# Performance work log

Hardware: AMD Instinct MI355X
Metric: run time of the kernel (lower is better)

The kernel has to match this reference:

```python
import jax, jax.numpy as jnp
import numpy as np

EPS = 1e-5

def _bn(x, g, b, m, v):
    # eval-mode batchnorm over channel axis 1 of NCHW
    scale = g * jax.lax.rsqrt(v + EPS)
    return x * scale[None, :, None, None] + (b - m * scale)[None, :, None, None]

def _dwconv3x3(x, w):
    # x: [N,C,H,W], w: [C,1,3,3] depthwise, stride 1, pad 1
    C = x.shape[1]
    return jax.lax.conv_general_dilated(
        x, w, window_strides=(1, 1), padding=((1, 1), (1, 1)),
        dimension_numbers=('NCHW', 'OIHW', 'NCHW'), feature_group_count=C)

def setup_inputs() -> dict:
    key = jax.random.key(0)
    ks = jax.random.split(key, 16)
    N, C, H, W = 32, 96, 56, 56
    Hd = 576  # hidden_dim = round(96 * 6)
    inp = {}
    inp['x'] = jax.random.normal(ks[0], (N, C, H, W), jnp.float32)
    inp['w1'] = jax.random.normal(ks[1], (Hd, C), jnp.float32) * 0.05
    inp['g1'] = jax.random.uniform(ks[2], (Hd,), jnp.float32, 0.5, 1.5)
    inp['b1'] = jax.random.normal(ks[3], (Hd,), jnp.float32) * 0.1
    inp['m1'] = jax.random.normal(ks[4], (Hd,), jnp.float32) * 0.1
    inp['v1'] = jax.random.uniform(ks[5], (Hd,), jnp.float32, 0.5, 1.5)
    inp['wdw'] = jax.random.normal(ks[6], (Hd, 1, 3, 3), jnp.float32) * 0.1
    inp['gdw'] = jax.random.uniform(ks[7], (Hd,), jnp.float32, 0.5, 1.5)
    inp['bdw'] = jax.random.normal(ks[8], (Hd,), jnp.float32) * 0.1
    inp['mdw'] = jax.random.normal(ks[9], (Hd,), jnp.float32) * 0.1
    inp['vdw'] = jax.random.uniform(ks[10], (Hd,), jnp.float32, 0.5, 1.5)
    inp['w2'] = jax.random.normal(ks[11], (C, Hd), jnp.float32) * 0.05
    inp['g2'] = jax.random.uniform(ks[12], (C,), jnp.float32, 0.5, 1.5)
    inp['b2'] = jax.random.normal(ks[13], (C,), jnp.float32) * 0.1
    inp['m2'] = jax.random.normal(ks[14], (C,), jnp.float32) * 0.1
    inp['v2'] = jax.random.uniform(ks[15], (C,), jnp.float32, 0.5, 1.5)
    return inp

def reference(x, w1, g1, b1, m1, v1, wdw, gdw, bdw, mdw, vdw, w2, g2, b2, m2, v2):
    # expand 1x1 conv (as GEMM) + BN + ReLU
    h = jnp.einsum('oc,bchw->bohw', w1, x)
    h = jax.nn.relu(_bn(h, g1, b1, m1, v1))
    # depthwise 3x3 + BN + ReLU
    h = _dwconv3x3(h, wdw)
    h = jax.nn.relu(_bn(h, gdw, bdw, mdw, vdw))
    # project 1x1 conv + BN (no ReLU)
    out = jnp.einsum('oc,bchw->bohw', w2, h)
    out = _bn(out, g2, b2, m2, v2)
    # residual (stride==1, inp==oup)
    return x + out
```

## Files before the change

kernel.cpp:

```cpp
#include <hip/hip_runtime.h>
#include <hip/hip_bf16.h>

typedef __attribute__((ext_vector_type(8))) short bf16x8;
typedef __attribute__((ext_vector_type(4))) float f32x4;
typedef unsigned short u16;
typedef unsigned int u32;

#define EPS 1e-5f
#define CIN 96
#define HD 576
#define HW 3136
#define NB 32

#define HCS   338
#define HC_OFF 0
#define H2_OFF 21632
#define H2S   40
#define SMEM_BYTES (H2_OFF + 224 * H2S * 2)

__device__ __forceinline__ u16 f2bf(float f) {
  u32 u = __builtin_bit_cast(u32, f);
  u32 r = u + 0x7fffu + ((u >> 16) & 1u);
  return (u16)(r >> 16);
}
__device__ __forceinline__ float bf2f(u16 h) {
  return __builtin_bit_cast(float, (u32)h << 16);
}

__global__ __launch_bounds__(256) void prep_kernel(
    const float* __restrict__ w1, const float* __restrict__ w2,
    const float* __restrict__ g1, const float* __restrict__ b1,
    const float* __restrict__ m1, const float* __restrict__ v1,
    const float* __restrict__ gdw, const float* __restrict__ bdw,
    const float* __restrict__ mdw, const float* __restrict__ vdw,
    const float* __restrict__ g2, const float* __restrict__ b2,
    const float* __restrict__ m2, const float* __restrict__ v2,
    u16* __restrict__ w1b, u16* __restrict__ w2b, float* __restrict__ bn)
{
  int i = blockIdx.x * 256 + threadIdx.x;
  if (i < HD * CIN) {
    w1b[i] = f2bf(w1[i]);
    w2b[i] = f2bf(w2[i]);
  }
  if (i < HD) {
    float s = g1[i] * rsqrtf(v1[i] + EPS);
    bn[i] = s;
    bn[HD + i] = b1[i] - m1[i] * s;
    float sd = gdw[i] * rsqrtf(vdw[i] + EPS);
    bn[2 * HD + i] = sd;
    bn[3 * HD + i] = bdw[i] - mdw[i] * sd;
  }
  if (i < CIN) {
    float s2 = g2[i] * rsqrtf(v2[i] + EPS);
    bn[4 * HD + i] = s2;
    bn[4 * HD + CIN + i] = b2[i] - m2[i] * s2;
  }
}

__global__ __launch_bounds__(448, 2) void fused_kernel(
    const float* __restrict__ x, const u16* __restrict__ w1b,
    const u16* __restrict__ w2b, const float* __restrict__ wdw,
    const float* __restrict__ bnp, float* __restrict__ out)
{
  extern __shared__ __align__(16) char smem[];
  u16* Hc  = (u16*)(smem + HC_OFF);
  u16* H2c = (u16*)(smem + H2_OFF);

  const int tid = threadIdx.x;
  const int r0  = blockIdx.x * 4;
  const int b   = blockIdx.y;
  const int l   = tid & 63;
  const int w   = tid >> 6;
  const int lr  = l & 15;
  const int kq  = l >> 4;
  const int kb  = kq * 8;

  const float* xb = x + (size_t)b * CIN * HW;
  const int pbase = (r0 - 1) * 56;
  bf16x8 xf[3][3];
#pragma unroll
  for (int t = 0; t < 3; ++t) {
    int gpx = pbase + (w * 3 + t) * 16 + lr;
    gpx = gpx < 0 ? 0 : (gpx > HW - 1 ? HW - 1 : gpx);
    const float* xp = xb + gpx;
#pragma unroll
    for (int ks = 0; ks < 3; ++ks) {
      bf16x8 pk;
#pragma unroll
      for (int j = 0; j < 8; ++j)
        pk[j] = (short)f2bf(xp[(size_t)(ks * 32 + kq * 8 + j) * HW]);
      xf[t][ks] = pk;
    }
  }

  const int chl_dw = tid & 31;
  const int cg_dw  = tid >> 5;
  f32x4 pacc[2][6] = {};

  for (int kc = 0; kc < 18; ++kc) {
    const int ch0 = kc * 32;

    const int gch_dw = ch0 + chl_dw;
    float wk[9];
#pragma unroll
    for (int k = 0; k < 9; ++k) wk[k] = wdw[gch_dw * 9 + k];
    const float sdw = bnp[2 * HD + gch_dw], hdw = bnp[3 * HD + gch_dw];

    bf16x8 af[2][3];
#pragma unroll
    for (int mt = 0; mt < 2; ++mt)
#pragma unroll
      for (int ks = 0; ks < 3; ++ks)
        af[mt][ks] = *(const bf16x8*)&w1b[(size_t)(ch0 + mt * 16 + lr) * CIN + ks * 32 + kb];

    f32x4 bsc[2], bsh[2];
#pragma unroll
    for (int mt = 0; mt < 2; ++mt) {
      bsc[mt] = *(const f32x4*)&bnp[ch0 + mt * 16 + kq * 4];
      bsh[mt] = *(const f32x4*)&bnp[HD + ch0 + mt * 16 + kq * 4];
    }

#pragma unroll
    for (int t = 0; t < 3; ++t) {
      f32x4 ea[2] = {};
#pragma unroll
      for (int ks = 0; ks < 3; ++ks) {
        ea[0] = __builtin_amdgcn_mfma_f32_16x16x32_bf16(af[0][ks], xf[t][ks], ea[0], 0, 0, 0);
        ea[1] = __builtin_amdgcn_mfma_f32_16x16x32_bf16(af[1][ks], xf[t][ks], ea[1], 0, 0, 0);
      }
      const int hpx = (w * 3 + t) * 16 + lr;
#pragma unroll
      for (int mt = 0; mt < 2; ++mt)
#pragma unroll
        for (int i = 0; i < 4; ++i) {
          int chl = mt * 16 + kq * 4 + i;
          float v = fmaxf(ea[mt][i] * bsc[mt][i] + bsh[mt][i], 0.f);
          Hc[chl * HCS + hpx] = f2bf(v);
        }
    }
    __syncthreads();

    {
      const int c0 = cg_dw * 4;
      float win[6][8];
#pragma unroll
      for (int hr = 0; hr < 6; ++hr) {
        int grow = r0 - 1 + hr;
        bool rv = (grow >= 0) && (grow < 56);
        const u16* rp = &Hc[chl_dw * HCS + hr * 56];
#pragma unroll
        for (int k2 = 0; k2 < 4; ++k2) {
          int cb = c0 - 2 + k2 * 2;
          u32 pr = (rv && cb >= 0) ? *(const u32*)(rp + cb) : 0u;
          win[hr][k2 * 2]     = bf2f((u16)pr);
          win[hr][k2 * 2 + 1] = bf2f((u16)(pr >> 16));
        }
        if (c0 + 4 >= 56) win[hr][6] = 0.f;
      }
#pragma unroll
      for (int orr = 0; orr < 4; ++orr) {
        float a4[4] = {0.f, 0.f, 0.f, 0.f};
#pragma unroll
        for (int dy = 0; dy < 3; ++dy)
#pragma unroll
          for (int j = 0; j < 4; ++j)
#pragma unroll
            for (int dx = 0; dx < 3; ++dx)
              a4[j] += wk[dy * 3 + dx] * win[orr + dy][j + dx + 1];
#pragma unroll
        for (int j = 0; j < 4; ++j) {
          float v = fmaxf(a4[j] * sdw + hdw, 0.f);
          H2c[(orr * 56 + c0 + j) * H2S + chl_dw] = f2bf(v);
        }
      }
    }
    __syncthreads();

    bf16x8 pa[6];
#pragma unroll
    for (int mt = 0; mt < 6; ++mt)
      pa[mt] = *(const bf16x8*)&w2b[(size_t)(mt * 16 + lr) * HD + ch0 + kb];
#pragma unroll
    for (int ntl = 0; ntl < 2; ++ntl) {
      int pt = w * 2 + ntl;
      bf16x8 pb = *(const bf16x8*)&H2c[(pt * 16 + lr) * H2S + kb];
#pragma unroll
      for (int mt = 0; mt < 6; ++mt)
        pacc[ntl][mt] = __builtin_amdgcn_mfma_f32_16x16x32_bf16(pa[mt], pb, pacc[ntl][mt], 0, 0, 0);
    }
  }

  const float* xr = x   + (size_t)b * CIN * HW + r0 * 56;
  float*       ob = out + (size_t)b * CIN * HW + r0 * 56;
#pragma unroll
  for (int mt = 0; mt < 6; ++mt) {
    f32x4 s2 = *(const f32x4*)&bnp[4 * HD + mt * 16 + kq * 4];
    f32x4 h2 = *(const f32x4*)&bnp[4 * HD + CIN + mt * 16 + kq * 4];
#pragma unroll
    for (int ntl = 0; ntl < 2; ++ntl) {
      int opx = (w * 2 + ntl) * 16 + lr;
#pragma unroll
      for (int i = 0; i < 4; ++i) {
        int c = mt * 16 + kq * 4 + i;
        float v = pacc[ntl][mt][i] * s2[i] + h2[i];
        size_t idx = (size_t)c * HW + opx;
        ob[idx] = v + xr[idx];
      }
    }
  }
}

extern "C" void kernel_launch(void* const* d_in, const int* in_sizes, int n_in,
                              void* d_out, int out_size, void* d_ws, size_t ws_size,
                              hipStream_t stream) {
  const float* x   = (const float*)d_in[0];
  const float* w1  = (const float*)d_in[1];
  const float* g1  = (const float*)d_in[2];
  const float* b1  = (const float*)d_in[3];
  const float* m1  = (const float*)d_in[4];
  const float* v1  = (const float*)d_in[5];
  const float* wdw = (const float*)d_in[6];
  const float* gdw = (const float*)d_in[7];
  const float* bdw = (const float*)d_in[8];
  const float* mdw = (const float*)d_in[9];
  const float* vdw = (const float*)d_in[10];
  const float* w2  = (const float*)d_in[11];
  const float* g2  = (const float*)d_in[12];
  const float* b2  = (const float*)d_in[13];
  const float* m2  = (const float*)d_in[14];
  const float* v2  = (const float*)d_in[15];
  float* out = (float*)d_out;

  char* ws = (char*)d_ws;
  u16*   w1b = (u16*)ws;
  u16*   w2b = (u16*)(ws + 2 * (size_t)HD * CIN);
  float* bnp = (float*)(ws + 4 * (size_t)HD * CIN);

  prep_kernel<<<dim3((HD * CIN + 255) / 256), 256, 0, stream>>>(
      w1, w2, g1, b1, m1, v1, gdw, bdw, mdw, vdw, g2, b2, m2, v2, w1b, w2b, bnp);

  fused_kernel<<<dim3(14, NB), 448, SMEM_BYTES, stream>>>(x, w1b, w2b, wdw, bnp, out);
}
```

Baseline: 259.5 us.

## Double output rows per block to cut halo recompute and reshape projection tiling

Each block now produces 8 output rows instead of 4, with 768 threads (12 waves), so the expand GEMM recomputes one halo row on each side for 8 rows rather than 4. This cuts redundant expand-conv work. The depthwise stage uses a rolling three-row register window, with only 448 threads active. The projection GEMM is re-tiled so each wave owns one 16-channel M tile across 14 pixel tiles. The costs are a larger LDS footprint (about 73 KB), fewer blocks (224), idle threads during the depthwise phase, and higher register pressure under launch_bounds(768,3).

Result: faster. 241.4 us (-7.0%).

```diff
diff --git a/kernel.cpp b/kernel.cpp
--- a/kernel.cpp
+++ b/kernel.cpp
@@ -12,11 +12,11 @@
 #define HW 3136
 #define NB 32
 
-#define HCS   338
+#define HCS   578
 #define HC_OFF 0
-#define H2_OFF 21632
+#define H2_OFF 36992
 #define H2S   40
-#define SMEM_BYTES (H2_OFF + 224 * H2S * 2)
+#define SMEM_BYTES (H2_OFF + 448 * H2S * 2)
 
 __device__ __forceinline__ u16 f2bf(float f) {
   u32 u = __builtin_bit_cast(u32, f);
@@ -57,7 +57,7 @@
   }
 }
 
-__global__ __launch_bounds__(448, 2) void fused_kernel(
+__global__ __launch_bounds__(768, 3) void fused_kernel(
     const float* __restrict__ x, const u16* __restrict__ w1b,
     const u16* __restrict__ w2b, const float* __restrict__ wdw,
     const float* __restrict__ bnp, float* __restrict__ out)
@@ -67,7 +67,7 @@
   u16* H2c = (u16*)(smem + H2_OFF);
 
   const int tid = threadIdx.x;
-  const int r0  = blockIdx.x * 4;
+  const int r0  = blockIdx.x * 8;
   const int b   = blockIdx.y;
   const int l   = tid & 63;
   const int w   = tid >> 6;
@@ -93,18 +93,25 @@
     }
   }
 
+  const bool dw_act = tid < 448;
   const int chl_dw = tid & 31;
   const int cg_dw  = tid >> 5;
-  f32x4 pacc[2][6] = {};
+  const int mi = w >> 1;
+  const int nj = w & 1;
+  f32x4 pacc[14] = {};
 
   for (int kc = 0; kc < 18; ++kc) {
     const int ch0 = kc * 32;
 
-    const int gch_dw = ch0 + chl_dw;
     float wk[9];
-#pragma unroll
-    for (int k = 0; k < 9; ++k) wk[k] = wdw[gch_dw * 9 + k];
-    const float sdw = bnp[2 * HD + gch_dw], hdw = bnp[3 * HD + gch_dw];
+    float sdw = 0.f, hdw = 0.f;
+    if (dw_act) {
+      const int gch_dw = ch0 + chl_dw;
+#pragma unroll
+      for (int k = 0; k < 9; ++k) wk[k] = wdw[gch_dw * 9 + k];
+      sdw = bnp[2 * HD + gch_dw];
+      hdw = bnp[3 * HD + gch_dw];
+    }
 
     bf16x8 af[2][3];
 #pragma unroll
@@ -140,72 +147,72 @@
     }
     __syncthreads();
 
-    {
+    if (dw_act) {
       const int c0 = cg_dw * 4;
-      float win[6][8];
-#pragma unroll
-      for (int hr = 0; hr < 6; ++hr) {
-        int grow = r0 - 1 + hr;
-        bool rv = (grow >= 0) && (grow < 56);
-        const u16* rp = &Hc[chl_dw * HCS + hr * 56];
-#pragma unroll
-        for (int k2 = 0; k2 < 4; ++k2) {
-          int cb = c0 - 2 + k2 * 2;
-          u32 pr = (rv && cb >= 0) ? *(const u32*)(rp + cb) : 0u;
-          win[hr][k2 * 2]     = bf2f((u16)pr);
-          win[hr][k2 * 2 + 1] = bf2f((u16)(pr >> 16));
+      const u16* hrow = &Hc[chl_dw * HCS];
+      float wr[3][8];
+
+#define LOADROW(slot, hr_)                                                  \
+      {                                                                     \
+        int grow = r0 - 1 + (hr_);                                          \
+        bool rv = (unsigned)grow < 56u;                                     \
+        const u16* rp = hrow + (hr_) * 56;                                  \
+        _Pragma("unroll")                                                   \
+        for (int k2 = 0; k2 < 4; ++k2) {                                    \
+          int cb = c0 - 2 + k2 * 2;                                         \
+          u32 pr = (rv && cb >= 0) ? *(const u32*)(rp + cb) : 0u;           \
+          wr[slot][k2 * 2]     = bf2f((u16)pr);                             \
+          wr[slot][k2 * 2 + 1] = bf2f((u16)(pr >> 16));                     \
+        }                                                                   \
+        if (c0 + 4 >= 56) wr[slot][6] = 0.f;                                \
+      }
+
+      LOADROW(0, 0)
+      LOADROW(1, 1)
+#pragma unroll
+      for (int orr = 0; orr < 8; ++orr) {
+        LOADROW((orr + 2) % 3, orr + 2)
+        float a4[4] = {0.f, 0.f, 0.f, 0.f};
+#pragma unroll
+        for (int dy = 0; dy < 3; ++dy) {
+          const int slot = (orr + dy) % 3;
+#pragma unroll
+          for (int j = 0; j < 4; ++j)
+#pragma unroll
+            for (int dx = 0; dx < 3; ++dx)
+              a4[j] += wk[dy * 3 + dx] * wr[slot][j + dx + 1];
         }
-        if (c0 + 4 >= 56) win[hr][6] = 0.f;
-      }
-#pragma unroll
-      for (int orr = 0; orr < 4; ++orr) {
-        float a4[4] = {0.f, 0.f, 0.f, 0.f};
-#pragma unroll
-        for (int dy = 0; dy < 3; ++dy)
-#pragma unroll
-          for (int j = 0; j < 4; ++j)
-#pragma unroll
-            for (int dx = 0; dx < 3; ++dx)
-              a4[j] += wk[dy * 3 + dx] * win[orr + dy][j + dx + 1];
 #pragma unroll
         for (int j = 0; j < 4; ++j) {
           float v = fmaxf(a4[j] * sdw + hdw, 0.f);
           H2c[(orr * 56 + c0 + j) * H2S + chl_dw] = f2bf(v);
         }
       }
+#undef LOADROW
     }
     __syncthreads();
 
-    bf16x8 pa[6];
-#pragma unroll
-    for (int mt = 0; mt < 6; ++mt)
-      pa[mt] = *(const bf16x8*)&w2b[(size_t)(mt * 16 + lr) * HD + ch0 + kb];
-#pragma unroll
-    for (int ntl = 0; ntl < 2; ++ntl) {
-      int pt = w * 2 + ntl;
-      bf16x8 pb = *(const bf16x8*)&H2c[(pt * 16 + lr) * H2S + kb];
-#pragma unroll
-      for (int mt = 0; mt < 6; ++mt)
-        pacc[ntl][mt] = __builtin_amdgcn_mfma_f32_16x16x32_bf16(pa[mt], pb, pacc[ntl][mt], 0, 0, 0);
+    bf16x8 pa = *(const bf16x8*)&w2b[(size_t)(mi * 16 + lr) * HD + ch0 + kb];
+#pragma unroll
+    for (int t = 0; t < 14; ++t) {
+      bf16x8 pb = *(const bf16x8*)&H2c[((nj * 14 + t) * 16 + lr) * H2S + kb];
+      pacc[t] = __builtin_amdgcn_mfma_f32_16x16x32_bf16(pa, pb, pacc[t], 0, 0, 0);
     }
   }
 
   const float* xr = x   + (size_t)b * CIN * HW + r0 * 56;
   float*       ob = out + (size_t)b * CIN * HW + r0 * 56;
-#pragma unroll
-  for (int mt = 0; mt < 6; ++mt) {
-    f32x4 s2 = *(const f32x4*)&bnp[4 * HD + mt * 16 + kq * 4];
-    f32x4 h2 = *(const f32x4*)&bnp[4 * HD + CIN + mt * 16 + kq * 4];
-#pragma unroll
-    for (int ntl = 0; ntl < 2; ++ntl) {
-      int opx = (w * 2 + ntl) * 16 + lr;
-#pragma unroll
-      for (int i = 0; i < 4; ++i) {
-        int c = mt * 16 + kq * 4 + i;
-        float v = pacc[ntl][mt][i] * s2[i] + h2[i];
-        size_t idx = (size_t)c * HW + opx;
-        ob[idx] = v + xr[idx];
-      }
+  f32x4 s2 = *(const f32x4*)&bnp[4 * HD + mi * 16 + kq * 4];
+  f32x4 h2 = *(const f32x4*)&bnp[4 * HD + CIN + mi * 16 + kq * 4];
+#pragma unroll
+  for (int t = 0; t < 14; ++t) {
+    int opx = (nj * 14 + t) * 16 + lr;
+#pragma unroll
+    for (int i = 0; i < 4; ++i) {
+      int c = mi * 16 + kq * 4 + i;
+      float v = pacc[t][i] * s2[i] + h2[i];
+      size_t idx = (size_t)c * HW + opx;
+      ob[idx] = v + xr[idx];
     }
   }
 }
@@ -236,8 +243,11 @@
   u16*   w2b = (u16*)(ws + 2 * (size_t)HD * CIN);
   float* bnp = (float*)(ws + 4 * (size_t)HD * CIN);
 
+  (void)hipFuncSetAttribute((const void*)fused_kernel,
+                            hipFuncAttributeMaxDynamicSharedMemorySize, SMEM_BYTES);
+
   prep_kernel<<<dim3((HD * CIN + 255) / 256), 256, 0, stream>>>(
       w1, w2, g1, b1, m1, v1, gdw, bdw, mdw, vdw, g2, b2, m2, v2, w1b, w2b, bnp);
 
-  fused_kernel<<<dim3(14, NB), 448, SMEM_BYTES, stream>>>(x, w1b, w2b, wdw, bnp, out);
-}
+  fused_kernel<<<dim3(7, NB), 768, SMEM_BYTES, stream>>>(x, w1b, w2b, wdw, bnp, out);
+}
```
